# Performance work log

Hardware: AMD Instinct MI355X
Metric: run time of the kernel (lower is better)

The kernel has to match this reference:

```python
import jax, jax.numpy as jnp
import numpy as np

WEIGHT = 0.1  # HISCLoss weight


def _gram(X):
    # linear kernel (the module's 'rbf' branch computes X @ Y.T)
    X = X.reshape(X.shape[0], -1)
    return X @ X.T  # [B, B]


def _center(K):
    # H K H with H = I - 11^T/B  ==  K - rowmean - colmean + grandmean
    rm = K.mean(axis=1, keepdims=True)
    cm = K.mean(axis=0, keepdims=True)
    gm = K.mean()
    return K - rm - cm + gm


def _hsic(X, Y):
    B = X.shape[0]
    Kc = _center(_gram(X))
    Lc = _center(_gram(Y))
    # trace(Kc @ Lc) without the B^3 matmul
    tr = jnp.einsum('ij,ji->', Kc, Lc)
    return tr / ((B - 1) ** 2)


def setup_inputs() -> dict:
    key = jax.random.key(0)
    ks = jax.random.split(key, 4)
    B, d = 4096, 256
    return {
        'e0': jax.random.normal(ks[0], (B, d), dtype=jnp.float32),
        'e1': jax.random.normal(ks[1], (B, d), dtype=jnp.float32),
        'e2': jax.random.normal(ks[2], (B, d), dtype=jnp.float32),
        'e3': jax.random.normal(ks[3], (B, d), dtype=jnp.float32),
    }


def reference(e0, e1, e2, e3):
    experts = [e0, e1, e2, e3]
    n = len(experts)
    vals = []
    for i in range(n):
        for j in range(i + 1, n):
            vals.append(_hsic(experts[i], experts[j]))
    L_hsic = jnp.mean(jnp.stack(vals))
    return WEIGHT * L_hsic
```

## Files before the change

kernel.cpp:

```cpp
#include <hip/hip_runtime.h>
#include <hip/hip_bf16.h>

#define B_ROWS 4096
#define DIM 256
#define NPAIR 6
#define PITCH 4160
#define BK 256
#define APITCH 264
#define KSPLIT 8
#define KCHUNK (B_ROWS / KSPLIT)

typedef short bf16x8 __attribute__((ext_vector_type(8)));
typedef float f32x4 __attribute__((ext_vector_type(4)));

__device__ __forceinline__ const float* sel(const float* e0, const float* e1,
                                            const float* e2, const float* e3, int i) {
    return i == 0 ? e0 : (i == 1 ? e1 : (i == 2 ? e2 : e3));
}

__device__ __forceinline__ int pair_i(int p) { return p < 3 ? 0 : (p < 5 ? 1 : 2); }
__device__ __forceinline__ int pair_j(int p) { return p < 3 ? p + 1 : (p < 5 ? p - 1 : 3); }

__device__ __forceinline__ unsigned short f32_to_bf16_rne(float f) {
    unsigned int u = __float_as_uint(f);
    unsigned int r = (u + 0x7FFFu + ((u >> 16) & 1u)) >> 16;
    return (unsigned short)r;
}


__global__ __launch_bounds__(256) void transpose_bf16_kernel(
        const float* __restrict__ e0, const float* __restrict__ e1,
        const float* __restrict__ e2, const float* __restrict__ e3,
        unsigned short* __restrict__ XT, float* __restrict__ sums_p) {
    int rt = blockIdx.x;
    int ct = blockIdx.y;
    int e  = blockIdx.z;
    const float* X = sel(e0, e1, e2, e3, e);
    unsigned short* XTe = XT + (size_t)e * DIM * PITCH;

    __shared__ float T[64][65];

    int t = threadIdx.x;
    int c4 = (t & 15) << 2;
    #pragma unroll
    for (int p = 0; p < 4; ++p) {
        int r = (t >> 4) + 16 * p;
        float4 v = *(const float4*)&X[(size_t)(rt * 64 + r) * DIM + ct * 64 + c4];
        T[c4 + 0][r] = v.x;
        T[c4 + 1][r] = v.y;
        T[c4 + 2][r] = v.z;
        T[c4 + 3][r] = v.w;
    }
    __syncthreads();

    #pragma unroll
    for (int p = 0; p < 2; ++p) {
        int id = 256 * p + t;
        int c = id >> 3;
        int roff = (id & 7) * 8;
        bf16x8 outv;
        float s8 = 0.f;
        #pragma unroll
        for (int s = 0; s < 8; ++s) {
            float f = T[c][roff + s];
            outv[s] = (short)f32_to_bf16_rne(f);
            s8 += f;
        }
        *(bf16x8*)&XTe[(size_t)(ct * 64 + c) * PITCH + rt * 64 + roff] = outv;
        s8 += __shfl_down(s8, 4, 8);
        s8 += __shfl_down(s8, 2, 8);
        s8 += __shfl_down(s8, 1, 8);
        if ((id & 7) == 0)
            sums_p[((size_t)(e * DIM + ct * 64 + c)) * 64 + rt] = s8;
    }
}

__global__ __launch_bounds__(512) void gram_v7_kernel(
        const unsigned short* __restrict__ XT, const float* __restrict__ sums_p,
        float* __restrict__ part) {
    __shared__ __align__(16) unsigned short smem[2 * 32 * APITCH];
    unsigned short* As = smem;
    unsigned short* Bs = smem + 32 * APITCH;
    float* red = (float*)smem;
    __shared__ float sA[32];
    __shared__ float sB[32];
    __shared__ float wsum[8];

    int blk = blockIdx.x;
    int p = blk >> 6;
    int tile = blk & 63;
    int a0 = (tile >> 3) * 32;
    int b0 = (tile & 7) * 32;
    int pi = pair_i(p), pj = pair_j(p);
    const unsigned short* Xp = XT + (size_t)pi * DIM * PITCH;
    const unsigned short* Yp = XT + (size_t)pj * DIM * PITCH;

    int tid = threadIdx.x;
    int w = tid >> 6;
    int L = tid & 63;

    int srow = tid >> 5;
    int soff = (tid & 31) * 8;
    const unsigned short* gA0 = Xp + (size_t)(a0 + srow) * PITCH + soff;
    const unsigned short* gA1 = Xp + (size_t)(a0 + 16 + srow) * PITCH + soff;
    const unsigned short* gB0 = Yp + (size_t)(b0 + srow) * PITCH + soff;
    const unsigned short* gB1 = Yp + (size_t)(b0 + 16 + srow) * PITCH + soff;
    int lA0 = srow * APITCH + soff;
    int lA1 = (16 + srow) * APITCH + soff;

    bf16x8 ra0 = *(const bf16x8*)gA0;
    bf16x8 ra1 = *(const bf16x8*)gA1;
    bf16x8 rb0 = *(const bf16x8*)gB0;
    bf16x8 rb1 = *(const bf16x8*)gB1;

    f32x4 acc[2][2] = {};
    int koff = w * 32 + (L >> 4) * 8;
    int frA0 = (L & 15) * APITCH + koff;
    int frA1 = (16 + (L & 15)) * APITCH + koff;

    for (int c = 0; c < 16; ++c) {
        __syncthreads();
        *(bf16x8*)&As[lA0] = ra0;
        *(bf16x8*)&As[lA1] = ra1;
        *(bf16x8*)&Bs[lA0] = rb0;
        *(bf16x8*)&Bs[lA1] = rb1;
        int cn = (c < 15) ? (c + 1) * BK : 0;
        ra0 = *(const bf16x8*)(gA0 + cn);
        ra1 = *(const bf16x8*)(gA1 + cn);
        rb0 = *(const bf16x8*)(gB0 + cn);
        rb1 = *(const bf16x8*)(gB1 + cn);
        __syncthreads();
        bf16x8 a0f = *(const bf16x8*)&As[frA0];
        bf16x8 a1f = *(const bf16x8*)&As[frA1];
        bf16x8 b0f = *(const bf16x8*)&Bs[frA0];
        bf16x8 b1f = *(const bf16x8*)&Bs[frA1];
        acc[0][0] = __builtin_amdgcn_mfma_f32_16x16x32_bf16(a0f, b0f, acc[0][0], 0, 0, 0);
        acc[0][1] = __builtin_amdgcn_mfma_f32_16x16x32_bf16(a0f, b1f, acc[0][1], 0, 0, 0);
        acc[1][0] = __builtin_amdgcn_mfma_f32_16x16x32_bf16(a1f, b0f, acc[1][0], 0, 0, 0);
        acc[1][1] = __builtin_amdgcn_mfma_f32_16x16x32_bf16(a1f, b1f, acc[1][1], 0, 0, 0);
    }

    __syncthreads();

    #pragma unroll
    for (int ti = 0; ti < 2; ++ti)
        #pragma unroll
        for (int tj = 0; tj < 2; ++tj)
            #pragma unroll
            for (int r = 0; r < 4; ++r) {
                int m = ti * 16 + (L >> 4) * 4 + r;
                int n = tj * 16 + (L & 15);
                red[w * 1056 + m * 33 + n] = acc[ti][tj][r];
            }

    {
        int fl = tid >> 4;
        int pr = tid & 15;
        float4 va = *(const float4*)&sums_p[((size_t)(pi * DIM + a0 + fl)) * 64 + pr * 4];
        float4 vb = *(const float4*)&sums_p[((size_t)(pj * DIM + b0 + fl)) * 64 + pr * 4];
        float sa = va.x + va.y + va.z + va.w;
        float sb = vb.x + vb.y + vb.z + vb.w;
        sa += __shfl_down(sa, 8, 16);
        sa += __shfl_down(sa, 4, 16);
        sa += __shfl_down(sa, 2, 16);
        sa += __shfl_down(sa, 1, 16);
        sb += __shfl_down(sb, 8, 16);
        sb += __shfl_down(sb, 4, 16);
        sb += __shfl_down(sb, 2, 16);
        sb += __shfl_down(sb, 1, 16);
        if (pr == 0) { sA[fl] = sa; sB[fl] = sb; }
    }
    __syncthreads();

    const float inv_b = 1.0f / (float)B_ROWS;
    float local = 0.f;
    #pragma unroll
    for (int q = 0; q < 2; ++q) {
        int pos = tid + q * 512;
        int m = pos >> 5, n = pos & 31;
        float s = 0.f;
        #pragma unroll
        for (int ww = 0; ww < 8; ++ww) s += red[ww * 1056 + m * 33 + n];
        float v = s - sA[m] * sB[n] * inv_b;
        local = fmaf(v, v, local);
    }
    #pragma unroll
    for (int off = 32; off > 0; off >>= 1) local += __shfl_down(local, off, 64);
    if (L == 0) wsum[w] = local;
    __syncthreads();
    if (tid == 0) {
        float s = 0.f;
        #pragma unroll
        for (int ww = 0; ww < 8; ++ww) s += wsum[ww];
        part[blk] = s;
    }
}

__global__ __launch_bounds__(512) void finalize384_kernel(
        const float* __restrict__ part, float* __restrict__ out) {
    int t = threadIdx.x;
    float local = (t < NPAIR * 64) ? part[t] : 0.f;
    #pragma unroll
    for (int off = 32; off > 0; off >>= 1) local += __shfl_down(local, off, 64);
    __shared__ float ws2[8];
    if ((t & 63) == 0) ws2[t >> 6] = local;
    __syncthreads();
    if (t == 0) {
        float s = 0.f;
        #pragma unroll
        for (int ww = 0; ww < 8; ++ww) s += ws2[ww];
        const float scale = 0.1f / (6.0f * 4095.0f * 4095.0f);
        out[0] = s * scale;
    }
}

__global__ void finalize_kernel(const float* __restrict__ acc, float* __restrict__ out) {
    if (threadIdx.x == 0) {
        const float scale = 0.1f / (6.0f * 4095.0f * 4095.0f);
        out[0] = acc[0] * scale;
    }
}


__global__ void col_sums_kernel(const float* __restrict__ e0, const float* __restrict__ e1,
                                const float* __restrict__ e2, const float* __restrict__ e3,
                                float* __restrict__ sums) {
    int e = blockIdx.y;
    const float* X = sel(e0, e1, e2, e3, e);
    int c = threadIdx.x;
    int r0 = blockIdx.x * 128;
    float s = 0.f;
    #pragma unroll 4
    for (int r = r0; r < r0 + 128; ++r) s += X[r * DIM + c];
    atomicAdd(&sums[e * DIM + c], s);
}

__global__ __launch_bounds__(256) void gram_kernel(
        const float* __restrict__ e0, const float* __restrict__ e1,
        const float* __restrict__ e2, const float* __restrict__ e3,
        float* __restrict__ G) {
    int kc = blockIdx.x;
    int tile = blockIdx.y;
    int p = blockIdx.z;
    const float* X = sel(e0, e1, e2, e3, pair_i(p));
    const float* Y = sel(e0, e1, e2, e3, pair_j(p));
    int a0 = (tile >> 2) * 64;
    int b0 = (tile & 3) * 64;
    int k0 = kc * KCHUNK;
    __shared__ float As[16][64];
    __shared__ float Bs[16][64];
    int lid = threadIdx.x;
    int lr = lid >> 4;
    int lc = (lid & 15) << 2;
    int ty = lid >> 4;
    int tx = lid & 15;
    float acc[4][4] = {};
    for (int ks = 0; ks < KCHUNK; ks += 16) {
        int row = k0 + ks + lr;
        float4 av = *(const float4*)&X[row * DIM + a0 + lc];
        float4 bv = *(const float4*)&Y[row * DIM + b0 + lc];
        __syncthreads();
        *(float4*)&As[lr][lc] = av;
        *(float4*)&Bs[lr][lc] = bv;
        __syncthreads();
        #pragma unroll
        for (int k = 0; k < 16; ++k) {
            float a[4], b[4];
            *(float4*)a = *(const float4*)&As[k][ty * 4];
            *(float4*)b = *(const float4*)&Bs[k][tx * 4];
            #pragma unroll
            for (int i = 0; i < 4; ++i)
                #pragma unroll
                for (int j = 0; j < 4; ++j)
                    acc[i][j] = fmaf(a[i], b[j], acc[i][j]);
        }
    }
    float* Gp = G + p * (DIM * DIM);
    #pragma unroll
    for (int i = 0; i < 4; ++i)
        #pragma unroll
        for (int j = 0; j < 4; ++j)
            atomicAdd(&Gp[(a0 + ty * 4 + i) * DIM + (b0 + tx * 4 + j)], acc[i][j]);
}

__global__ void reduce_kernel(const float* __restrict__ G, const float* __restrict__ sums,
                              float* __restrict__ acc) {
    float local = 0.f;
    const int total = NPAIR * DIM * DIM;
    for (int idx = blockIdx.x * blockDim.x + threadIdx.x; idx < total;
         idx += gridDim.x * blockDim.x) {
        int p = idx >> 16;
        int ab = idx & 65535;
        int a = ab >> 8;
        int b = ab & 255;
        float v = G[idx] - sums[pair_i(p) * DIM + a] * sums[pair_j(p) * DIM + b] * (1.0f / (float)B_ROWS);
        local = fmaf(v, v, local);
    }
    #pragma unroll
    for (int off = 32; off > 0; off >>= 1) local += __shfl_down(local, off, 64);
    __shared__ float wsum[4];
    if ((threadIdx.x & 63) == 0) wsum[threadIdx.x >> 6] = local;
    __syncthreads();
    if (threadIdx.x == 0) {
        float s = wsum[0] + wsum[1] + wsum[2] + wsum[3];
        atomicAdd(acc, s);
    }
}


extern "C" void kernel_launch(void* const* d_in, const int* in_sizes, int n_in,
                              void* d_out, int out_size, void* d_ws, size_t ws_size,
                              hipStream_t stream) {
    const float* e0 = (const float*)d_in[0];
    const float* e1 = (const float*)d_in[1];
    const float* e2 = (const float*)d_in[2];
    const float* e3 = (const float*)d_in[3];

    size_t need = 266240 + (size_t)4 * DIM * PITCH * sizeof(unsigned short);

    if (ws_size >= need) {
        float* sums_p = (float*)d_ws;
        float* part = (float*)((char*)d_ws + 262144);
        unsigned short* XT = (unsigned short*)((char*)d_ws + 266240);
        transpose_bf16_kernel<<<dim3(64, 4, 4), 256, 0, stream>>>(e0, e1, e2, e3, XT, sums_p);
        gram_v7_kernel<<<NPAIR * 64, 512, 0, stream>>>(XT, sums_p, part);
        finalize384_kernel<<<1, 512, 0, stream>>>(part, (float*)d_out);
    } else {
        float* sums = (float*)d_ws;
        float* acc  = (float*)((char*)d_ws + 4096);
        float* G = (float*)((char*)d_ws + 8192);
        size_t zbytes = 8192 + (size_t)NPAIR * DIM * DIM * sizeof(float);
        hipMemsetAsync(d_ws, 0, zbytes, stream);
        col_sums_kernel<<<dim3(32, 4), 256, 0, stream>>>(e0, e1, e2, e3, sums);
        gram_kernel<<<dim3(KSPLIT, 16, NPAIR), 256, 0, stream>>>(e0, e1, e2, e3, G);
        reduce_kernel<<<384, 256, 0, stream>>>(G, sums, acc);
        finalize_kernel<<<1, 64, 0, stream>>>(acc, (float*)d_out);
    }
}
```

Measured before the change: 86.00 us.

## Use direct global-to-LDS loads with double buffering and XOR swizzle in gram kernel

The gram kernel now uses global_load_lds to copy bf16 tiles straight into shared memory instead of staging them through registers. LDS is double-buffered so the next K chunk loads while MFMAs run on the current one, and each loop iteration needs one barrier instead of two. An XOR swizzle replaces the padded pitch to avoid bank conflicts. LDS use grows to 64KB per block, which may reduce occupancy, and the async LDS writes depend on the barrier for correct waiting.

After: 85.29 us. Within noise of the previous version (-0.8%).

```diff
diff --git a/kernel.cpp b/kernel.cpp
--- a/kernel.cpp
+++ b/kernel.cpp
@@ -6,7 +6,6 @@
 #define NPAIR 6
 #define PITCH 4160
 #define BK 256
-#define APITCH 264
 #define KSPLIT 8
 #define KCHUNK (B_ROWS / KSPLIT)
 
@@ -25,6 +24,12 @@
     unsigned int u = __float_as_uint(f);
     unsigned int r = (u + 0x7FFFu + ((u >> 16) & 1u)) >> 16;
     return (unsigned short)r;
+}
+
+__device__ __forceinline__ void glds16(const void* g, void* l) {
+    __builtin_amdgcn_global_load_lds(
+        (const __attribute__((address_space(1))) unsigned int*)(g),
+        (__attribute__((address_space(3))) unsigned int*)(l), 16, 0, 0);
 }
 
 
@@ -75,16 +80,11 @@
     }
 }
 
-__global__ __launch_bounds__(512) void gram_v7_kernel(
+__global__ __launch_bounds__(512) void gram_v8_kernel(
         const unsigned short* __restrict__ XT, const float* __restrict__ sums_p,
         float* __restrict__ part) {
-    __shared__ __align__(16) unsigned short smem[2 * 32 * APITCH];
-    unsigned short* As = smem;
-    unsigned short* Bs = smem + 32 * APITCH;
-    float* red = (float*)smem;
-    __shared__ float sA[32];
-    __shared__ float sB[32];
-    __shared__ float wsum[8];
+    __shared__ __align__(16) unsigned short smem[2 * 64 * 256];
+    char* base = (char*)smem;
 
     int blk = blockIdx.x;
     int p = blk >> 6;
@@ -100,47 +100,52 @@
     int L = tid & 63;
 
     int srow = tid >> 5;
-    int soff = (tid & 31) * 8;
-    const unsigned short* gA0 = Xp + (size_t)(a0 + srow) * PITCH + soff;
-    const unsigned short* gA1 = Xp + (size_t)(a0 + 16 + srow) * PITCH + soff;
-    const unsigned short* gB0 = Yp + (size_t)(b0 + srow) * PITCH + soff;
-    const unsigned short* gB1 = Yp + (size_t)(b0 + 16 + srow) * PITCH + soff;
-    int lA0 = srow * APITCH + soff;
-    int lA1 = (16 + srow) * APITCH + soff;
-
-    bf16x8 ra0 = *(const bf16x8*)gA0;
-    bf16x8 ra1 = *(const bf16x8*)gA1;
-    bf16x8 rb0 = *(const bf16x8*)gB0;
-    bf16x8 rb1 = *(const bf16x8*)gB1;
+    int soffb = (tid & 31) * 16;
+    int swzb = soffb ^ ((srow & 7) << 4);
+    const unsigned short* gA0 = Xp + (size_t)(a0 + srow) * PITCH + (swzb >> 1);
+    const unsigned short* gA1 = Xp + (size_t)(a0 + 16 + srow) * PITCH + (swzb >> 1);
+    const unsigned short* gB0 = Yp + (size_t)(b0 + srow) * PITCH + (swzb >> 1);
+    const unsigned short* gB1 = Yp + (size_t)(b0 + 16 + srow) * PITCH + (swzb >> 1);
+    int lp0 = tid * 16;
+    int lp1 = 8192 + tid * 16;
+
+    int rA = L & 15;
+    int koffb = w * 64 + (L >> 4) * 16;
+    int fr0 = rA * 512 + (koffb ^ ((rA & 7) << 4));
 
     f32x4 acc[2][2] = {};
-    int koff = w * 32 + (L >> 4) * 8;
-    int frA0 = (L & 15) * APITCH + koff;
-    int frA1 = (16 + (L & 15)) * APITCH + koff;
+
+    glds16(gA0, base + lp0);
+    glds16(gA1, base + lp1);
+    glds16(gB0, base + 16384 + lp0);
+    glds16(gB1, base + 16384 + lp1);
+    __syncthreads();
 
     for (int c = 0; c < 16; ++c) {
-        __syncthreads();
-        *(bf16x8*)&As[lA0] = ra0;
-        *(bf16x8*)&As[lA1] = ra1;
-        *(bf16x8*)&Bs[lA0] = rb0;
-        *(bf16x8*)&Bs[lA1] = rb1;
-        int cn = (c < 15) ? (c + 1) * BK : 0;
-        ra0 = *(const bf16x8*)(gA0 + cn);
-        ra1 = *(const bf16x8*)(gA1 + cn);
-        rb0 = *(const bf16x8*)(gB0 + cn);
-        rb1 = *(const bf16x8*)(gB1 + cn);
-        __syncthreads();
-        bf16x8 a0f = *(const bf16x8*)&As[frA0];
-        bf16x8 a1f = *(const bf16x8*)&As[frA1];
-        bf16x8 b0f = *(const bf16x8*)&Bs[frA0];
-        bf16x8 b1f = *(const bf16x8*)&Bs[frA1];
+        if (c < 15) {
+            int cn = (c + 1) * BK;
+            char* Ab = base + ((c + 1) & 1) * 32768;
+            glds16(gA0 + cn, Ab + lp0);
+            glds16(gA1 + cn, Ab + lp1);
+            glds16(gB0 + cn, Ab + 16384 + lp0);
+            glds16(gB1 + cn, Ab + 16384 + lp1);
+        }
+        const char* Ar = base + (c & 1) * 32768;
+        bf16x8 a0f = *(const bf16x8*)(Ar + fr0);
+        bf16x8 a1f = *(const bf16x8*)(Ar + 8192 + fr0);
+        bf16x8 b0f = *(const bf16x8*)(Ar + 16384 + fr0);
+        bf16x8 b1f = *(const bf16x8*)(Ar + 16384 + 8192 + fr0);
         acc[0][0] = __builtin_amdgcn_mfma_f32_16x16x32_bf16(a0f, b0f, acc[0][0], 0, 0, 0);
         acc[0][1] = __builtin_amdgcn_mfma_f32_16x16x32_bf16(a0f, b1f, acc[0][1], 0, 0, 0);
         acc[1][0] = __builtin_amdgcn_mfma_f32_16x16x32_bf16(a1f, b0f, acc[1][0], 0, 0, 0);
         acc[1][1] = __builtin_amdgcn_mfma_f32_16x16x32_bf16(a1f, b1f, acc[1][1], 0, 0, 0);
-    }
-
-    __syncthreads();
+        __syncthreads();
+    }
+
+    float* red  = (float*)base;
+    float* sA   = (float*)(base + 33792);
+    float* sB   = (float*)(base + 33920);
+    float* wsum = (float*)(base + 34048);
 
     #pragma unroll
     for (int ti = 0; ti < 2; ++ti)
@@ -323,7 +328,7 @@
         float* part = (float*)((char*)d_ws + 262144);
         unsigned short* XT = (unsigned short*)((char*)d_ws + 266240);
         transpose_bf16_kernel<<<dim3(64, 4, 4), 256, 0, stream>>>(e0, e1, e2, e3, XT, sums_p);
-        gram_v7_kernel<<<NPAIR * 64, 512, 0, stream>>>(XT, sums_p, part);
+        gram_v8_kernel<<<NPAIR * 64, 512, 0, stream>>>(XT, sums_p, part);
         finalize384_kernel<<<1, 512, 0, stream>>>(part, (float*)d_out);
     } else {
         float* sums = (float*)d_ws;
```
